# Kernel tuning notes

Measured on AMD Instinct MI355X. Metric: run time of the kernel, lower is better.

Reference implementation:

```python
import jax, jax.numpy as jnp
import numpy as np

# Model constants (from init_kwargs)
NF, NC, E, B = 100000, 4000, 500000, 256
D_FACT, D_COMP = 1536, 27
HIDDEN, HEADS, CPH = 128, 4, 32  # out_per_head = hidden // heads
NUM_LAYERS = 2
TIME_DIM = 8
T_SCALE = 30.0
EDGE_DIM = 2 + TIME_DIM  # [sentiment, decay, time2vec]
ATTN_SCALE = 1.0  # 1 / attn_temperature
NEG_SLOPE = 0.2


def time_edge_features(ea, lam):
    # ea: [E, 2] = [sentiment, decay]; second column in [0,1] -> decay branch
    s = jnp.clip(ea[:, 0:1], -1.0, 1.0)
    decay = jnp.clip(ea[:, 1:2], 0.0, 1.0)
    lam = jnp.maximum(lam, 1e-6)
    delta_t = -jnp.log(jnp.maximum(decay, 1e-6)) / lam
    t = jnp.log1p(jnp.maximum(delta_t, 0.0)) / T_SCALE  # [E,1]
    freqs = jnp.arange(1, TIME_DIM, dtype=ea.dtype)      # [TIME_DIM-1]
    sins = jnp.sin(t * freqs)                            # [E,TIME_DIM-1]
    return jnp.concatenate([s, decay, sins, t], axis=-1)  # [E, EDGE_DIM]


def seg_softmax(logits, seg, n):
    # logits: [E,H]; softmax over edges sharing the same destination node
    m = jax.ops.segment_max(logits, seg, num_segments=n)
    z = jnp.exp(logits - m[seg])
    den = jax.ops.segment_sum(z, seg, num_segments=n)
    return z / (den[seg] + 1e-16)


def seg_mean(x, seg, n):
    s = jax.ops.segment_sum(x, seg, num_segments=n)
    cnt = jax.ops.segment_sum(jnp.ones((x.shape[0],), x.dtype), seg, num_segments=n)
    return s / jnp.maximum(cnt, 1.0)[:, None]


def layernorm(x, g, b, eps=1e-5):
    mu = jnp.mean(x, axis=-1, keepdims=True)
    var = jnp.var(x, axis=-1, keepdims=True)
    return (x - mu) * jax.lax.rsqrt(var + eps) * g + b


def setup_inputs() -> dict:
    key = jax.random.key(0)
    ks = jax.random.split(key, 32)

    x_fact = jax.random.normal(ks[0], (NF, D_FACT), jnp.float32)
    x_company = jax.random.normal(ks[1], (NC, D_COMP), jnp.float32)
    u = jax.random.uniform(ks[2], (E, 2), jnp.float32)
    edge_attr = jnp.concatenate([u[:, 0:1] * 2.0 - 1.0, u[:, 1:2]], axis=1)
    edge_index = jnp.stack([
        jax.random.randint(ks[3], (E,), 0, NF),
        jax.random.randint(ks[4], (E,), 0, NC),
    ]).astype(jnp.int32)
    batch_fact = jnp.sort(jax.random.randint(ks[5], (NF,), 0, B)).astype(jnp.int32)
    batch_company = jnp.sort(jax.random.randint(ks[6], (NC,), 0, B)).astype(jnp.int32)

    def p(k, shape):
        return jax.random.normal(k, shape, jnp.float32) * 0.05

    inp = dict(
        x_fact=x_fact, x_company=x_company, edge_attr=edge_attr,
        edge_index=edge_index, batch_fact=batch_fact, batch_company=batch_company,
        lambda_decay=jnp.array(0.01, jnp.float32),
        Wf=p(ks[7], (D_FACT, HIDDEN)), bf=jnp.zeros((HIDDEN,), jnp.float32),
        Wc=p(ks[8], (D_COMP, HIDDEN)), bc=jnp.zeros((HIDDEN,), jnp.float32),
        Wl=p(ks[9], (NUM_LAYERS, HIDDEN, HIDDEN)), bl=jnp.zeros((NUM_LAYERS, HIDDEN), jnp.float32),
        Wr=p(ks[10], (NUM_LAYERS, HIDDEN, HIDDEN)), br=jnp.zeros((NUM_LAYERS, HIDDEN), jnp.float32),
        We=p(ks[11], (NUM_LAYERS, EDGE_DIM, HIDDEN)), be=jnp.zeros((NUM_LAYERS, HIDDEN), jnp.float32),
        att=p(ks[12], (NUM_LAYERS, HEADS, CPH)),
        bias_out=jnp.zeros((NUM_LAYERS, HIDDEN), jnp.float32),
        ln_g=jnp.ones((NUM_LAYERS, HIDDEN), jnp.float32), ln_b=jnp.zeros((NUM_LAYERS, HIDDEN), jnp.float32),
        Wg=p(ks[13], (2 * HIDDEN, 1)), bg=jnp.zeros((1,), jnp.float32),
        W1=p(ks[14], (HIDDEN, HIDDEN)), b1=jnp.zeros((HIDDEN,), jnp.float32),
        W2=p(ks[15], (HIDDEN, 1)), b2=jnp.zeros((1,), jnp.float32),
    )
    return inp


def reference(x_fact, x_company, edge_attr, edge_index, batch_fact, batch_company,
              lambda_decay, Wf, bf, Wc, bc, Wl, bl, Wr, br, We, be, att, bias_out,
              ln_g, ln_b, Wg, bg, W1, b1, W2, b2):
    src, dst = edge_index[0], edge_index[1]
    ef = time_edge_features(edge_attr, lambda_decay)          # [E, EDGE_DIM]

    # per-node-type input encoders
    hf = jax.nn.relu(x_fact @ Wf + bf)                         # [NF, H]
    hc = jax.nn.relu(x_company @ Wc + bc)                      # [NC, H]
    n_c = x_company.shape[0]

    for l in range(NUM_LAYERS):
        # GATv2 (edge-conditioned, bipartite fact->company, share_weights=False)
        gl = (hf @ Wl[l] + bl[l]).reshape(-1, HEADS, CPH)      # src transform [NF,H,C]
        gr = (hc @ Wr[l] + br[l]).reshape(-1, HEADS, CPH)      # dst transform [NC,H,C]
        ge = (ef @ We[l] + be[l]).reshape(-1, HEADS, CPH)      # edge transform [E,H,C]
        e = jax.nn.leaky_relu(gl[src] + gr[dst] + ge, NEG_SLOPE)  # [E,H,C]
        logits = jnp.einsum('ehc,hc->eh', e, att[l]) * ATTN_SCALE  # [E,H]
        alpha = seg_softmax(logits, dst, n_c)                   # scatter-softmax over dst
        msg = alpha[..., None] * gl[src]                        # [E,H,C]
        out = jax.ops.segment_sum(msg, dst, num_segments=n_c).reshape(n_c, HIDDEN) + bias_out[l]
        hc = layernorm(hc + jax.nn.relu(out), ln_g[l], ln_b[l])  # residual + post-norm

    # gated readout over graphs in batch
    pf = seg_mean(hf, batch_fact, B)                            # [B,H]
    pc = seg_mean(hc, batch_company, B)                         # [B,H]
    g = jax.nn.sigmoid(jnp.concatenate([pf, pc], axis=-1) @ Wg + bg)  # [B,1]
    h = g * pf + (1.0 - g) * pc                                 # [B,H]
    logit = jax.nn.relu(h @ W1 + b1) @ W2 + b2                  # [B,1]
    return logit
```

## Files before the change

kernel.cpp:

```cpp
#include <hip/hip_runtime.h>
#include <hip/hip_bf16.h>
#include <hip/hip_fp16.h>
#include <math.h>

#define NFAC 100000
#define NCOMP 4000
#define NEDGE 500000
#define NB 256
#define DF 1536
#define DC 27
#define H 128
#define EDIM 10
#define EDIMP 16

typedef __attribute__((ext_vector_type(8))) short short8v;
typedef __attribute__((ext_vector_type(4))) float f32x4;

#define GLOAD_LDS16(g, l)                                                              \
  __builtin_amdgcn_global_load_lds((const __attribute__((address_space(1))) unsigned int*)(g), \
                                   (__attribute__((address_space(3))) unsigned int*)(l), 16, 0, 0)

__device__ __forceinline__ float group32_sum(float v) {
#pragma unroll
  for (int m = 16; m > 0; m >>= 1) v += __shfl_xor(v, m);
  return v;
}

__device__ __forceinline__ unsigned short bf16rn(float x) {
  unsigned int u = __float_as_uint(x);
  unsigned int r = (u + 0x7fffu + ((u >> 16) & 1u)) >> 16;
  return (unsigned short)r;
}
__device__ __forceinline__ float bf16tof(unsigned short h) {
  return __uint_as_float(((unsigned int)h) << 16);
}

__global__ void k_edge_feat(const float* __restrict__ ea, const float* __restrict__ lamp,
                            float* __restrict__ ef) {
  int e = blockIdx.x * blockDim.x + threadIdx.x;
  if (e >= NEDGE) return;
  float s   = fminf(fmaxf(ea[2 * e], -1.f), 1.f);
  float dec = fminf(fmaxf(ea[2 * e + 1], 0.f), 1.f);
  float lam = fmaxf(lamp[0], 1e-6f);
  float dt  = -logf(fmaxf(dec, 1e-6f)) / lam;
  float t   = log1pf(fmaxf(dt, 0.f)) * (1.f / 30.f);
  float* o = ef + (size_t)e * EDIMP;
  o[0] = s;
  o[1] = dec;
#pragma unroll
  for (int k = 1; k < 8; k++) o[1 + k] = __sinf(t * (float)k);
  o[9] = t;
  o[10] = 0.f; o[11] = 0.f; o[12] = 0.f; o[13] = 0.f; o[14] = 0.f; o[15] = 0.f;
}

__global__ void k_hist(const int* __restrict__ dst, int* __restrict__ deg) {
  int e = blockIdx.x * blockDim.x + threadIdx.x;
  if (e < NEDGE) atomicAdd(&deg[dst[e]], 1);
}

__global__ __launch_bounds__(1024) void k_scan(const int* __restrict__ deg, int* __restrict__ off) {
  __shared__ int s[4096];
  int t = threadIdx.x;
  for (int i = t; i < 4096; i += 1024) s[i] = (i < NCOMP) ? deg[i] : 0;
  __syncthreads();
  for (int d = 1; d < 4096; d <<= 1) {
    int vals[4];
#pragma unroll
    for (int j = 0; j < 4; j++) {
      int i = t + j * 1024;
      vals[j] = (i >= d) ? s[i - d] : 0;
    }
    __syncthreads();
#pragma unroll
    for (int j = 0; j < 4; j++) {
      int i = t + j * 1024;
      s[i] += vals[j];
    }
    __syncthreads();
  }
  for (int i = t; i < 4096; i += 1024) off[i + 1] = s[i];
  if (t == 0) off[0] = 0;
}

__global__ void k_scatter(const int* __restrict__ dst, const int* __restrict__ src,
                          const int* __restrict__ off, int* __restrict__ cur,
                          int* __restrict__ eid, int* __restrict__ srcs) {
  int e = blockIdx.x * blockDim.x + threadIdx.x;
  if (e < NEDGE) {
    int d = dst[e];
    int p = atomicAdd(&cur[d], 1);
    eid[off[d] + p] = e;
    srcs[off[d] + p] = src[e];
  }
}

__global__ void k_conv_w(const float* __restrict__ W, unsigned short* __restrict__ Bh,
                         unsigned short* __restrict__ Bl, int K) {
  int i = blockIdx.x * blockDim.x + threadIdx.x;
  if (i >= K * H) return;
  int k = i >> 7, c = i & 127;
  float x = W[i];
  unsigned short h = bf16rn(x);
  unsigned short l = bf16rn(x - bf16tof(h));
  Bh[(size_t)c * K + k] = h;
  Bl[(size_t)c * K + k] = l;
}

__global__ void k_conv_wl2(const float* __restrict__ Wl, unsigned short* __restrict__ Bh,
                           unsigned short* __restrict__ Bl) {
  int i = blockIdx.x * blockDim.x + threadIdx.x;
  if (i >= 2 * H * H) return;
  int l = i >> 14;
  int r = i & 16383;
  int k = r >> 7, c = r & 127;
  float x = Wl[i];
  unsigned short h = bf16rn(x);
  unsigned short lo = bf16rn(x - bf16tof(h));
  int col = c + 128 * l;
  Bh[(size_t)col * H + k] = h;
  Bl[(size_t)col * H + k] = lo;
}

__device__ __forceinline__ unsigned int packhi(unsigned int u1, unsigned int u0) {
  return __builtin_amdgcn_perm(u1, u0, 0x07060302u);
}

__device__ __forceinline__ void split8(const float4& a0, const float4& a1, short8v& ah,
                                       short8v& al) {
  float xs[8] = {a0.x, a0.y, a0.z, a0.w, a1.x, a1.y, a1.z, a1.w};
  unsigned int hu[8], lu[8];
#pragma unroll
  for (int j = 0; j < 8; j++) {
    unsigned int u = __float_as_uint(xs[j]);
    hu[j] = u & 0xffff0000u;
    lu[j] = __float_as_uint(xs[j] - __uint_as_float(hu[j]));
  }
  unsigned int hw[4], lw[4];
#pragma unroll
  for (int j = 0; j < 4; j++) {
    hw[j] = packhi(hu[2 * j + 1], hu[2 * j]);
    lw[j] = packhi(lu[2 * j + 1], lu[2 * j]);
  }
  ah = *(short8v*)hw;
  al = *(short8v*)lw;
}

__global__ __launch_bounds__(256, 2) void k_gemm_mfma(const float* __restrict__ A,
                                                      const unsigned short* __restrict__ Bth,
                                                      const unsigned short* __restrict__ Btl,
                                                      const float* __restrict__ bias,
                                                      float* __restrict__ C, int M, int K,
                                                      int dorelu) {
  __shared__ __align__(16) char smem[2][16384];
  int tid = threadIdx.x;
  int wave = tid >> 6, lane = tid & 63;
  int m0 = blockIdx.x * 128;
  int wm = (wave >> 1) * 64, wn = (wave & 1) * 64;
  int fr = lane & 15, fg = lane >> 4;
  int nIter = K >> 5;

  f32x4 acc[4][4];
#pragma unroll
  for (int i = 0; i < 4; i++)
#pragma unroll
    for (int j = 0; j < 4; j++) acc[i][j] = (f32x4){0.f, 0.f, 0.f, 0.f};

  int a_row = (lane >> 3);
  int a_s = lane & 7;

  const unsigned short* bhp[4];
  const unsigned short* blp[4];
#pragma unroll
  for (int nf = 0; nf < 4; nf++) {
    int col = wn + 16 * nf + fr;
    bhp[nf] = Bth + (size_t)col * K + fg * 8;
    blp[nf] = Btl + (size_t)col * K + fg * 8;
  }

  auto stageA = [&](int buf, int k0) {
    char* base = smem[buf];
#pragma unroll
    for (int q = 0; q < 4; q++) {
      int j = wave + 4 * q;
      int row = j * 8 + a_row;
      int grow = m0 + row;
      if (grow >= M) grow = 0;
      const float* src = A + (size_t)grow * K + k0 + ((a_s ^ (row & 7)) << 2);
      GLOAD_LDS16(src, base + j * 1024);
    }
  };

  stageA(0, 0);
  __syncthreads();

  for (int it = 0; it < nIter; ++it) {
    int cur = it & 1;
    int k0 = it << 5;
    short8v bh[4], bl[4];
#pragma unroll
    for (int nf = 0; nf < 4; nf++) {
      bh[nf] = *(const short8v*)(bhp[nf] + k0);
      bl[nf] = *(const short8v*)(blp[nf] + k0);
    }
    if (it + 1 < nIter) stageA(cur ^ 1, (it + 1) << 5);
    const char* cb = smem[cur];
    short8v ah[4], al[4];
#pragma unroll
    for (int mf = 0; mf < 4; mf++) {
      int r = wm + 16 * mf + fr;
      int s0 = (2 * fg) ^ (r & 7);
      int s1 = (2 * fg + 1) ^ (r & 7);
      float4 a0 = *(const float4*)(cb + r * 128 + s0 * 16);
      float4 a1 = *(const float4*)(cb + r * 128 + s1 * 16);
      split8(a0, a1, ah[mf], al[mf]);
    }
#pragma unroll
    for (int nf = 0; nf < 4; nf++) {
#pragma unroll
      for (int mf = 0; mf < 4; mf++) {
        acc[mf][nf] = __builtin_amdgcn_mfma_f32_16x16x32_bf16(ah[mf], bh[nf], acc[mf][nf], 0, 0, 0);
        acc[mf][nf] = __builtin_amdgcn_mfma_f32_16x16x32_bf16(ah[mf], bl[nf], acc[mf][nf], 0, 0, 0);
        acc[mf][nf] = __builtin_amdgcn_mfma_f32_16x16x32_bf16(al[mf], bh[nf], acc[mf][nf], 0, 0, 0);
      }
    }
    __syncthreads();
  }

#pragma unroll
  for (int mf = 0; mf < 4; mf++) {
    int rbase = m0 + wm + 16 * mf + 4 * fg;
#pragma unroll
    for (int nf = 0; nf < 4; nf++) {
      int col = wn + 16 * nf + fr;
      float bv = bias[col];
#pragma unroll
      for (int j = 0; j < 4; j++) {
        int row = rbase + j;
        if (row < M) {
          float v = acc[mf][nf][j] + bv;
          if (dorelu) v = fmaxf(v, 0.f);
          C[(size_t)row * H + col] = v;
        }
      }
    }
  }
}

__global__ __launch_bounds__(256, 2) void k_gemm_n256(const float* __restrict__ A,
                                                      const unsigned short* __restrict__ Bth,
                                                      const unsigned short* __restrict__ Btl,
                                                      const float* __restrict__ bias,
                                                      __half* __restrict__ C, int M) {
  __shared__ __align__(16) char smem[2][8192];
  const int K = 128;
  int tid = threadIdx.x;
  int wave = tid >> 6, lane = tid & 63;
  int m0 = blockIdx.x * 64;
  int wn = wave * 64;
  int fr = lane & 15, fg = lane >> 4;

  f32x4 acc[4][4];
#pragma unroll
  for (int i = 0; i < 4; i++)
#pragma unroll
    for (int j = 0; j < 4; j++) acc[i][j] = (f32x4){0.f, 0.f, 0.f, 0.f};

  int a_row = (lane >> 3);
  int a_s = lane & 7;

  const unsigned short* bhp[4];
  const unsigned short* blp[4];
#pragma unroll
  for (int nf = 0; nf < 4; nf++) {
    int col = wn + 16 * nf + fr;
    bhp[nf] = Bth + (size_t)col * K + fg * 8;
    blp[nf] = Btl + (size_t)col * K + fg * 8;
  }

  auto stageA = [&](int buf, int k0) {
    char* base = smem[buf];
#pragma unroll
    for (int q = 0; q < 2; q++) {
      int j = wave + 4 * q;
      int row = j * 8 + a_row;
      int grow = m0 + row;
      if (grow >= M) grow = 0;
      GLOAD_LDS16(A + (size_t)grow * K + k0 + ((a_s ^ (row & 7)) << 2), base + j * 1024);
    }
  };

  stageA(0, 0);
  __syncthreads();

  for (int it = 0; it < 4; ++it) {
    int cur = it & 1;
    int k0 = it << 5;
    short8v bh[4], bl[4];
#pragma unroll
    for (int nf = 0; nf < 4; nf++) {
      bh[nf] = *(const short8v*)(bhp[nf] + k0);
      bl[nf] = *(const short8v*)(blp[nf] + k0);
    }
    if (it + 1 < 4) stageA(cur ^ 1, (it + 1) << 5);
    const char* cb = smem[cur];
    short8v ah[4], al[4];
#pragma unroll
    for (int mf = 0; mf < 4; mf++) {
      int r = 16 * mf + fr;
      int s0 = (2 * fg) ^ (r & 7);
      int s1 = (2 * fg + 1) ^ (r & 7);
      float4 a0 = *(const float4*)(cb + r * 128 + s0 * 16);
      float4 a1 = *(const float4*)(cb + r * 128 + s1 * 16);
      split8(a0, a1, ah[mf], al[mf]);
    }
#pragma unroll
    for (int nf = 0; nf < 4; nf++) {
#pragma unroll
      for (int mf = 0; mf < 4; mf++) {
        acc[mf][nf] = __builtin_amdgcn_mfma_f32_16x16x32_bf16(ah[mf], bh[nf], acc[mf][nf], 0, 0, 0);
        acc[mf][nf] = __builtin_amdgcn_mfma_f32_16x16x32_bf16(ah[mf], bl[nf], acc[mf][nf], 0, 0, 0);
        acc[mf][nf] = __builtin_amdgcn_mfma_f32_16x16x32_bf16(al[mf], bh[nf], acc[mf][nf], 0, 0, 0);
      }
    }
    __syncthreads();
  }

#pragma unroll
  for (int mf = 0; mf < 4; mf++) {
    int rbase = m0 + 16 * mf + 4 * fg;
#pragma unroll
    for (int nf = 0; nf < 4; nf++) {
      int col = wn + 16 * nf + fr;
      float bv = bias[col];
#pragma unroll
      for (int j = 0; j < 4; j++) {
        int row = rbase + j;
        if (row < M) C[(size_t)row * 256 + col] = __float2half(acc[mf][nf][j] + bv);
      }
    }
  }
}

__global__ void k_enc_comp(const float* __restrict__ X, const float* __restrict__ Wc,
                           const float* __restrict__ bc, float* __restrict__ hc) {
  int tid = threadIdx.x;
  int r = blockIdx.x * 2 + (tid >> 7);
  int j = tid & 127;
  if (r >= NCOMP) return;
  float acc = bc[j];
  const float* x = X + (size_t)r * DC;
#pragma unroll
  for (int k = 0; k < DC; k++) acc = fmaf(x[k], Wc[k * H + j], acc);
  hc[(size_t)r * H + j] = fmaxf(acc, 0.f);
}

__global__ __launch_bounds__(128) void k_node2(
    const __half* __restrict__ gl2, const float* __restrict__ ef, const int* __restrict__ srcs,
    const int* __restrict__ csr_off, const int* __restrict__ csr_eid,
    const float* __restrict__ Wr, const float* __restrict__ br, const float* __restrict__ We,
    const float* __restrict__ be, const float* __restrict__ att,
    const float* __restrict__ bias_out, const float* __restrict__ lng,
    const float* __restrict__ lnb, float* __restrict__ hc) {
  int v = blockIdx.x;
  int t = threadIdx.x;
  __shared__ float hcs[H];
  __shared__ float red[2], redq[2];
  float x = hc[(size_t)v * H + t];
  hcs[t] = x;
  int e0 = csr_off[v], e1 = csr_off[v + 1];
  __syncthreads();

  float y = x;
#pragma unroll 1
  for (int l = 0; l < 2; l++) {
    const float* Wrl = Wr + (size_t)l * H * H;
    float wre[EDIM];
#pragma unroll
    for (int k = 0; k < EDIM; k++) wre[k] = We[l * EDIM * H + k * H + t];
    float attv = att[l * H + t];
    float bev = be[l * H + t];
    float grv = br[l * H + t];
    for (int k = 0; k < H; k++) grv = fmaf(hcs[k], Wrl[k * H + t], grv);
    float grb = grv + bev;
    const __half* gl = gl2 + l * 128;

    float m = -INFINITY, s = 0.f, acc = 0.f;
    int i = e0;
    int eid = 0, sid = 0;
    if (i < e1) {
      eid = csr_eid[i];
      sid = srcs[i];
    }
    while (i < e1) {
      float glv = __half2float(gl[(size_t)sid * 256 + t]);
      const float* efr = ef + (size_t)eid * EDIMP;
      float4 f0 = *(const float4*)(efr);
      float4 f1 = *(const float4*)(efr + 4);
      float2 f2 = *(const float2*)(efr + 8);
      int ni = i + 1;
      if (ni < e1) {
        eid = csr_eid[ni];
        sid = srcs[ni];
      }
      float ge = grb;
      ge = fmaf(f0.x, wre[0], ge);
      ge = fmaf(f0.y, wre[1], ge);
      ge = fmaf(f0.z, wre[2], ge);
      ge = fmaf(f0.w, wre[3], ge);
      ge = fmaf(f1.x, wre[4], ge);
      ge = fmaf(f1.y, wre[5], ge);
      ge = fmaf(f1.z, wre[6], ge);
      ge = fmaf(f1.w, wre[7], ge);
      ge = fmaf(f2.x, wre[8], ge);
      ge = fmaf(f2.y, wre[9], ge);
      float ev = glv + ge;
      ev = ev > 0.f ? ev : 0.2f * ev;
      float logit = group32_sum(ev * attv);
      if (logit > m) {
        float scale = __expf(m - logit);
        s = s * scale + 1.f;
        acc = acc * scale + glv;
        m = logit;
      } else {
        float z = __expf(logit - m);
        s += z;
        acc = fmaf(z, glv, acc);
      }
      i = ni;
    }
    float outv = acc / (s + 1e-16f);
    outv += bias_out[l * H + t];
    outv = fmaxf(outv, 0.f);
    y = x + outv;
    float sv = y, qv = y * y;
#pragma unroll
    for (int mm = 32; mm > 0; mm >>= 1) {
      sv += __shfl_xor(sv, mm);
      qv += __shfl_xor(qv, mm);
    }
    int wid = t >> 6, lane = t & 63;
    if (lane == 0) {
      red[wid] = sv;
      redq[wid] = qv;
    }
    __syncthreads();
    float mean = (red[0] + red[1]) * (1.f / H);
    float var = (redq[0] + redq[1]) * (1.f / H) - mean * mean;
    float r = rsqrtf(var + 1e-5f);
    y = (y - mean) * r * lng[l * H + t] + lnb[l * H + t];
    hcs[t] = y;
    x = y;
    __syncthreads();
  }
  hc[(size_t)v * H + t] = y;
}

template <int CHUNK>
__global__ __launch_bounds__(128) void k_segmean(const float* __restrict__ X,
                                                 const int* __restrict__ seg, int n,
                                                 float* __restrict__ sum, int* __restrict__ cnt) {
  int t = threadIdx.x;
  int n0 = blockIdx.x * CHUNK;
  int n1 = min(n0 + CHUNK, n);
  float acc = 0.f;
  int c = 0;
  int curs = -1;
  for (int i = n0; i < n1; ++i) {
    int sg = seg[i];
    if (sg != curs) {
      if (curs >= 0) {
        atomicAdd(&sum[(size_t)curs * H + t], acc);
        if (t == 0) atomicAdd(&cnt[curs], c);
      }
      curs = sg;
      acc = 0.f;
      c = 0;
    }
    acc += X[(size_t)i * H + t];
    c++;
  }
  if (curs >= 0) {
    atomicAdd(&sum[(size_t)curs * H + t], acc);
    if (t == 0) atomicAdd(&cnt[curs], c);
  }
}

__global__ __launch_bounds__(128) void k_readout(const float* __restrict__ pf,
                                                 const float* __restrict__ pc,
                                                 const int* __restrict__ cf,
                                                 const int* __restrict__ cc,
                                                 const float* __restrict__ Wg,
                                                 const float* __restrict__ bg,
                                                 const float* __restrict__ W1,
                                                 const float* __restrict__ b1,
                                                 const float* __restrict__ W2,
                                                 const float* __restrict__ b2,
                                                 float* __restrict__ out) {
  int b = blockIdx.x, t = threadIdx.x;
  __shared__ float hs[H];
  __shared__ float red[2], red2[2];
  int wid = t >> 6, lane = t & 63;
  float nf = fmaxf((float)cf[b], 1.f);
  float nc = fmaxf((float)cc[b], 1.f);
  float pfv = pf[(size_t)b * H + t] / nf;
  float pcv = pc[(size_t)b * H + t] / nc;
  float gp = pfv * Wg[t] + pcv * Wg[H + t];
  float sv = gp;
#pragma unroll
  for (int mm = 32; mm > 0; mm >>= 1) sv += __shfl_xor(sv, mm);
  if (lane == 0) red[wid] = sv;
  __syncthreads();
  float g = 1.f / (1.f + expf(-(red[0] + red[1] + bg[0])));
  float h = g * pfv + (1.f - g) * pcv;
  hs[t] = h;
  __syncthreads();
  float a = b1[t];
  for (int k = 0; k < H; k++) a = fmaf(hs[k], W1[k * H + t], a);
  a = fmaxf(a, 0.f);
  float p = a * W2[t];
#pragma unroll
  for (int mm = 32; mm > 0; mm >>= 1) p += __shfl_xor(p, mm);
  if (lane == 0) red2[wid] = p;
  __syncthreads();
  if (t == 0) out[b] = red2[0] + red2[1] + b2[0];
}

extern "C" void kernel_launch(void* const* d_in, const int* in_sizes, int n_in, void* d_out,
                              int out_size, void* d_ws, size_t ws_size, hipStream_t stream) {
  const float* x_fact = (const float*)d_in[0];
  const float* x_comp = (const float*)d_in[1];
  const float* ea = (const float*)d_in[2];
  const int* eidx = (const int*)d_in[3];
  const int* batf = (const int*)d_in[4];
  const int* batc = (const int*)d_in[5];
  const float* lam = (const float*)d_in[6];
  const float* Wf = (const float*)d_in[7];
  const float* bf = (const float*)d_in[8];
  const float* Wc = (const float*)d_in[9];
  const float* bc = (const float*)d_in[10];
  const float* Wl = (const float*)d_in[11];
  const float* bl = (const float*)d_in[12];
  const float* Wr = (const float*)d_in[13];
  const float* br_ = (const float*)d_in[14];
  const float* We = (const float*)d_in[15];
  const float* be = (const float*)d_in[16];
  const float* att = (const float*)d_in[17];
  const float* b_out = (const float*)d_in[18];
  const float* lng = (const float*)d_in[19];
  const float* lnb = (const float*)d_in[20];
  const float* Wg = (const float*)d_in[21];
  const float* bg = (const float*)d_in[22];
  const float* W1 = (const float*)d_in[23];
  const float* b1 = (const float*)d_in[24];
  const float* W2 = (const float*)d_in[25];
  const float* b2 = (const float*)d_in[26];
  float* out = (float*)d_out;

  char* w = (char*)d_ws;
  auto carve = [&](size_t bytes) -> char* {
    char* p = w;
    w += (bytes + 255) & ~(size_t)255;
    return p;
  };
  float* HF = (float*)carve((size_t)NFAC * H * 4);
  __half* GL2 = (__half*)carve((size_t)NFAC * 256 * 2);
  float* HC = (float*)carve((size_t)NCOMP * H * 4);
  float* EF = (float*)carve((size_t)NEDGE * EDIMP * 4);
  int* OFF = (int*)carve(4100 * 4);
  int* EID = (int*)carve((size_t)NEDGE * 4);
  int* SRCS = (int*)carve((size_t)NEDGE * 4);
  unsigned short* WfH = (unsigned short*)carve((size_t)DF * H * 2);
  unsigned short* WfL = (unsigned short*)carve((size_t)DF * H * 2);
  unsigned short* WlH2 = (unsigned short*)carve((size_t)256 * H * 2);
  unsigned short* WlL2 = (unsigned short*)carve((size_t)256 * H * 2);
  char* zbase = w;
  int* DEG = (int*)carve(4096 * 4);
  int* CUR = (int*)carve(4096 * 4);
  float* PF = (float*)carve((size_t)NB * H * 4);
  float* PC = (float*)carve((size_t)NB * H * 4);
  int* CF = (int*)carve(NB * 4);
  int* CC = (int*)carve(NB * 4);
  size_t zbytes = (size_t)(w - zbase);
  hipMemsetAsync(zbase, 0, zbytes, stream);

  const int* srcArr = eidx;
  const int* dstArr = eidx + NEDGE;

  k_edge_feat<<<(NEDGE + 255) / 256, 256, 0, stream>>>(ea, lam, EF);
  k_hist<<<(NEDGE + 255) / 256, 256, 0, stream>>>(dstArr, DEG);
  k_scan<<<1, 1024, 0, stream>>>(DEG, OFF);
  k_scatter<<<(NEDGE + 255) / 256, 256, 0, stream>>>(dstArr, srcArr, OFF, CUR, EID, SRCS);

  k_conv_w<<<(DF * H + 255) / 256, 256, 0, stream>>>(Wf, WfH, WfL, DF);
  k_conv_wl2<<<(2 * H * H + 255) / 256, 256, 0, stream>>>(Wl, WlH2, WlL2);

  k_gemm_mfma<<<(NFAC + 127) / 128, 256, 0, stream>>>(x_fact, WfH, WfL, bf, HF, NFAC, DF, 1);
  k_enc_comp<<<NCOMP / 2, 256, 0, stream>>>(x_comp, Wc, bc, HC);

  k_gemm_n256<<<(NFAC + 63) / 64, 256, 0, stream>>>(HF, WlH2, WlL2, bl, GL2, NFAC);

  k_node2<<<NCOMP, 128, 0, stream>>>(GL2, EF, SRCS, OFF, EID, Wr, br_, We, be, att, b_out, lng,
                                     lnb, HC);

  k_segmean<128><<<(NFAC + 127) / 128, 128, 0, stream>>>(HF, batf, NFAC, PF, CF);
  k_segmean<64><<<(NCOMP + 63) / 64, 128, 0, stream>>>(HC, batc, NCOMP, PC, CC);
  k_readout<<<NB, 128, 0, stream>>>(PF, PC, CF, CC, Wg, bg, W1, b1, W2, b2, out);
}
```

Before: 814.5 us.

## Split-K the fact encoder GEMM in two with a separate reduction kernel

The large x_fact x Wf GEMM is split along K into two halves using a second grid dimension. Each half writes raw fp32 partial sums into scratch buffers, and a new elementwise kernel adds the two partials plus bias and applies ReLU. The aim is more blocks and better CU balance for a grid that previously filled only about one and a half waves. The cost is an extra kernel launch and roughly 200 MB of additional partial-sum traffic, with one partial buffer reusing the GL2 workspace.

```diff
diff --git a/kernel.cpp b/kernel.cpp
--- a/kernel.cpp
+++ b/kernel.cpp
@@ -150,14 +150,17 @@
                                                       const unsigned short* __restrict__ Btl,
                                                       const float* __restrict__ bias,
                                                       float* __restrict__ C, int M, int K,
-                                                      int dorelu) {
+                                                      int dorelu, float* __restrict__ Cpart) {
   __shared__ __align__(16) char smem[2][16384];
   int tid = threadIdx.x;
   int wave = tid >> 6, lane = tid & 63;
   int m0 = blockIdx.x * 128;
   int wm = (wave >> 1) * 64, wn = (wave & 1) * 64;
   int fr = lane & 15, fg = lane >> 4;
-  int nIter = K >> 5;
+  int nsplit = gridDim.y;
+  int Ks = K / nsplit;
+  int kbeg = blockIdx.y * Ks;
+  int nIter = Ks >> 5;
 
   f32x4 acc[4][4];
 #pragma unroll
@@ -173,8 +176,8 @@
 #pragma unroll
   for (int nf = 0; nf < 4; nf++) {
     int col = wn + 16 * nf + fr;
-    bhp[nf] = Bth + (size_t)col * K + fg * 8;
-    blp[nf] = Btl + (size_t)col * K + fg * 8;
+    bhp[nf] = Bth + (size_t)col * K + kbeg + fg * 8;
+    blp[nf] = Btl + (size_t)col * K + kbeg + fg * 8;
   }
 
   auto stageA = [&](int buf, int k0) {
@@ -190,7 +193,7 @@
     }
   };
 
-  stageA(0, 0);
+  stageA(0, kbeg);
   __syncthreads();
 
   for (int it = 0; it < nIter; ++it) {
@@ -202,7 +205,7 @@
       bh[nf] = *(const short8v*)(bhp[nf] + k0);
       bl[nf] = *(const short8v*)(blp[nf] + k0);
     }
-    if (it + 1 < nIter) stageA(cur ^ 1, (it + 1) << 5);
+    if (it + 1 < nIter) stageA(cur ^ 1, kbeg + ((it + 1) << 5));
     const char* cb = smem[cur];
     short8v ah[4], al[4];
 #pragma unroll
@@ -226,24 +229,58 @@
     __syncthreads();
   }
 
-#pragma unroll
-  for (int mf = 0; mf < 4; mf++) {
-    int rbase = m0 + wm + 16 * mf + 4 * fg;
-#pragma unroll
-    for (int nf = 0; nf < 4; nf++) {
-      int col = wn + 16 * nf + fr;
-      float bv = bias[col];
-#pragma unroll
-      for (int j = 0; j < 4; j++) {
-        int row = rbase + j;
-        if (row < M) {
-          float v = acc[mf][nf][j] + bv;
-          if (dorelu) v = fmaxf(v, 0.f);
-          C[(size_t)row * H + col] = v;
+  if (nsplit == 1) {
+#pragma unroll
+    for (int mf = 0; mf < 4; mf++) {
+      int rbase = m0 + wm + 16 * mf + 4 * fg;
+#pragma unroll
+      for (int nf = 0; nf < 4; nf++) {
+        int col = wn + 16 * nf + fr;
+        float bv = bias[col];
+#pragma unroll
+        for (int j = 0; j < 4; j++) {
+          int row = rbase + j;
+          if (row < M) {
+            float v = acc[mf][nf][j] + bv;
+            if (dorelu) v = fmaxf(v, 0.f);
+            C[(size_t)row * H + col] = v;
+          }
         }
       }
     }
-  }
+  } else {
+    float* P = Cpart + (size_t)blockIdx.y * M * H;
+#pragma unroll
+    for (int mf = 0; mf < 4; mf++) {
+      int rbase = m0 + wm + 16 * mf + 4 * fg;
+#pragma unroll
+      for (int nf = 0; nf < 4; nf++) {
+        int col = wn + 16 * nf + fr;
+#pragma unroll
+        for (int j = 0; j < 4; j++) {
+          int row = rbase + j;
+          if (row < M) P[(size_t)row * H + col] = acc[mf][nf][j];
+        }
+      }
+    }
+  }
+}
+
+__global__ __launch_bounds__(256) void k_reduce2(const float* __restrict__ P0,
+                                                 const float* __restrict__ P1,
+                                                 const float* __restrict__ bias,
+                                                 float* __restrict__ C, int total4) {
+  int i = blockIdx.x * blockDim.x + threadIdx.x;
+  if (i >= total4) return;
+  float4 a = ((const float4*)P0)[i];
+  float4 b = ((const float4*)P1)[i];
+  float4 bv = ((const float4*)bias)[i & 31];
+  float4 r;
+  r.x = fmaxf(a.x + b.x + bv.x, 0.f);
+  r.y = fmaxf(a.y + b.y + bv.y, 0.f);
+  r.z = fmaxf(a.z + b.z + bv.z, 0.f);
+  r.w = fmaxf(a.w + b.w + bv.w, 0.f);
+  ((float4*)C)[i] = r;
 }
 
 __global__ __launch_bounds__(256, 2) void k_gemm_n256(const float* __restrict__ A,
@@ -563,7 +600,9 @@
     return p;
   };
   float* HF = (float*)carve((size_t)NFAC * H * 4);
-  __half* GL2 = (__half*)carve((size_t)NFAC * 256 * 2);
+  float* GL = (float*)carve((size_t)NFAC * H * 4);
+  float* CP1 = (float*)carve((size_t)NFAC * H * 4);
+  __half* GL2 = (__half*)GL;
   float* HC = (float*)carve((size_t)NCOMP * H * 4);
   float* EF = (float*)carve((size_t)NEDGE * EDIMP * 4);
   int* OFF = (int*)carve(4100 * 4);
@@ -594,7 +633,13 @@
   k_conv_w<<<(DF * H + 255) / 256, 256, 0, stream>>>(Wf, WfH, WfL, DF);
   k_conv_wl2<<<(2 * H * H + 255) / 256, 256, 0, stream>>>(Wl, WlH2, WlL2);
 
-  k_gemm_mfma<<<(NFAC + 127) / 128, 256, 0, stream>>>(x_fact, WfH, WfL, bf, HF, NFAC, DF, 1);
+  {
+    float* CPART = GL;
+    dim3 grid((NFAC + 127) / 128, 2);
+    k_gemm_mfma<<<grid, 256, 0, stream>>>(x_fact, WfH, WfL, bf, HF, NFAC, DF, 1, CPART);
+    int total4 = NFAC * H / 4;
+    k_reduce2<<<(total4 + 255) / 256, 256, 0, stream>>>(GL, CP1, bf, HF, total4);
+  }
   k_enc_comp<<<NCOMP / 2, 256, 0, stream>>>(x_comp, Wc, bc, HC);
 
   k_gemm_n256<<<(NFAC + 63) / 64, 256, 0, stream>>>(HF, WlH2, WlL2, bl, GL2, NFAC);
```

After: 831.6 us. 1.02x slower.
